# Kernel tuning notes

Measured on AMD Instinct MI355X. Metric: run time of the kernel, lower is better.

The kernel has to match this reference:

```python
import jax, jax.numpy as jnp
import numpy as np

HEADS = 16
LN_EPS = 1e-5


def setup_inputs() -> dict:
    key = jax.random.key(0)
    ks = jax.random.split(key, 4)
    B, S, C, U = 2, 2048, 1024, 1024
    scale = 1.0 / np.sqrt(C)
    return {
        "inputs": jax.random.normal(ks[0], (B, S, C), dtype=jnp.float32),
        "Wq": jax.random.normal(ks[1], (C, U), dtype=jnp.float32) * scale,
        "bq": jnp.zeros((U,), dtype=jnp.float32),
        "Wk": jax.random.normal(ks[2], (C, U), dtype=jnp.float32) * scale,
        "bk": jnp.zeros((U,), dtype=jnp.float32),
        "Wv": jax.random.normal(ks[3], (C, U), dtype=jnp.float32) * scale,
        "bv": jnp.zeros((U,), dtype=jnp.float32),
        "ln_gamma": jnp.ones((S, U), dtype=jnp.float32),
        "ln_beta": jnp.zeros((S, U), dtype=jnp.float32),
    }


def reference(inputs, Wq, bq, Wk, bk, Wv, bv, ln_gamma, ln_beta):
    B, S, C = inputs.shape
    U = Wq.shape[1]
    H = HEADS
    dh = U // H

    Q = inputs @ Wq + bq  # [B,S,U]
    K = inputs @ Wk + bk
    V = inputs @ Wv + bv

    # torch: concat(split(X, U//H, dim=-1), dim=0) -> head-major stacking on batch
    def split_heads(X):
        return jnp.moveaxis(X.reshape(B, S, H, dh), 2, 0).reshape(H * B, S, dh)

    Q_, K_, V_ = split_heads(Q), split_heads(K), split_heads(V)

    scores = jnp.einsum('bqd,bkd->bqk', Q_, K_) / jnp.sqrt(jnp.float32(dh))
    tri = jnp.tril(jnp.ones((S, S), dtype=bool))  # causal mask
    scores = jnp.where(tri[None, :, :], scores, jnp.float32(-1e9))
    attn = jax.nn.softmax(scores, axis=-1)
    out_ = jnp.einsum('bqk,bkd->bqd', attn, V_)  # [H*B,S,dh]

    # inverse: split on batch into H chunks of size B, concat on feature dim
    out = jnp.moveaxis(out_.reshape(H, B, S, dh), 0, 2).reshape(B, S, U)

    out = out + inputs  # residual

    # LayerNorm over normalized_shape=[S, U] (joint seq+feature stats)
    mu = jnp.mean(out, axis=(-2, -1), keepdims=True)
    var = jnp.mean(jnp.square(out - mu), axis=(-2, -1), keepdims=True)
    out = (out - mu) / jnp.sqrt(var + LN_EPS) * ln_gamma + ln_beta
    return out
```

## Files before the change

kernel.cpp:

```cpp
#include <hip/hip_runtime.h>
#include <hip/hip_bf16.h>


typedef __bf16 bf16_t;
typedef __bf16 bf16x8 __attribute__((ext_vector_type(8)));
typedef __bf16 bf16x4 __attribute__((ext_vector_type(4)));
typedef _Float16 f16_t;
typedef _Float16 f16x2 __attribute__((ext_vector_type(2)));
typedef _Float16 f16x4 __attribute__((ext_vector_type(4)));
typedef _Float16 f16x8 __attribute__((ext_vector_type(8)));
typedef float f32x4 __attribute__((ext_vector_type(4)));

constexpr int Bsz = 2;
constexpr int Seq = 2048;
constexpr int Cdim = 1024;
constexpr int Udim = 1024;
constexpr int Hn = 16;
constexpr int Dh = 64;
constexpr int Mrows = Bsz * Seq;
constexpr int PerBatch = Seq * Udim;
constexpr float SCLQ = 0.125f * 1.44269504088896340736f;

#if __has_builtin(__builtin_amdgcn_exp2f)
#define EXP2F(x) __builtin_amdgcn_exp2f(x)
#else
#define EXP2F(x) exp2f(x)
#endif

#define AINL __attribute__((always_inline))
#define BARRIER() __builtin_amdgcn_s_barrier()
#define SCHEDB() __builtin_amdgcn_sched_barrier(0)
#define WAITV4() asm volatile("s_waitcnt vmcnt(4)" ::: "memory")
#define WAITV0() asm volatile("s_waitcnt vmcnt(0)" ::: "memory")

__device__ __forceinline__ void gload16(const void* g, void* l)
{
    __builtin_amdgcn_global_load_lds(
        (const __attribute__((address_space(1))) void*)g,
        (__attribute__((address_space(3))) void*)l, 16, 0, 0);
}

__device__ __forceinline__ f16x2 pkrtz(float a, float b)
{
    return __builtin_bit_cast(f16x2, __builtin_amdgcn_cvt_pkrtz(a, b));
}

__global__ __launch_bounds__(256)
void prep(const float* __restrict__ X,
          const float* __restrict__ Wq, const float* __restrict__ Wk,
          const float* __restrict__ Wv,
          bf16_t* __restrict__ Xb,
          bf16_t* __restrict__ Tq, bf16_t* __restrict__ Tk,
          bf16_t* __restrict__ Tv, float* __restrict__ stats)
{
    int z = blockIdx.z;
    int tid = threadIdx.x;
    if (z < 3) {
        const float* W = (z == 0) ? Wq : (z == 1) ? Wk : Wv;
        bf16_t* T = (z == 0) ? Tq : (z == 1) ? Tk : Tv;
        __shared__ bf16_t t[64][65];
        int x0 = blockIdx.x * 64, y0 = blockIdx.y * 64;
        int tx = tid & 63, ty = tid >> 6;
        for (int i = ty; i < 64; i += 4)
            t[i][tx] = (bf16_t)W[(size_t)(y0 + i) * Cdim + x0 + tx];
        __syncthreads();
        for (int i = ty; i < 64; i += 4)
            T[(size_t)(x0 + i) * Cdim + y0 + tx] = t[tx][i];
    } else {
        int bi = blockIdx.y * 16 + blockIdx.x;
        if (bi == 0 && tid < 4) stats[tid] = 0.0f;
        const float4* Xv = (const float4*)X;
#pragma unroll
        for (int k = 0; k < 16; k++) {
            int i = bi * 4096 + k * 256 + tid;
            float4 v = Xv[i];
            bf16x4 o = { (bf16_t)v.x, (bf16_t)v.y, (bf16_t)v.z, (bf16_t)v.w };
            *(bf16x4*)(Xb + (size_t)i * 4) = o;
        }
    }
}

__global__ __launch_bounds__(256)
void gemm_qkv(const bf16_t* __restrict__ X,
              const bf16_t* __restrict__ Wt0, const bf16_t* __restrict__ Wt1,
              const bf16_t* __restrict__ Wt2,
              const float* __restrict__ b0, const float* __restrict__ b1,
              const float* __restrict__ b2,
              f16_t* __restrict__ O0, f16_t* __restrict__ O1, f16_t* __restrict__ O2v)
{
    int z = blockIdx.z;
    const bf16_t* Wt = (z == 0) ? Wt0 : (z == 1) ? Wt1 : Wt2;
    const float* bias = (z == 0) ? b0 : (z == 1) ? b1 : b2;
    float scl = (z == 0) ? SCLQ : 1.0f;

    constexpr int Kd = 1024, Nd = 1024;
    __shared__ __align__(16) bf16_t As[2][4096];
    __shared__ __align__(16) bf16_t Bs[2][4096];

    int tid = threadIdx.x;
    int wave = tid >> 6, lane = tid & 63, quad = lane >> 4, l16 = lane & 15;
    int wm = (wave & 1) * 64, wn = (wave >> 1) * 64;
    int m0 = blockIdx.y * 128, n0 = blockIdx.x * 128;

    f32x4 acc[4][4] = {};

    int e0 = wave * 512 + lane * 8;
    int r0 = e0 >> 5, c0 = e0 & 31;
    int e1 = e0 + 2048;
    int r1 = e1 >> 5, c1 = e1 & 31;
    const bf16_t* Ag = X + (size_t)m0 * Kd;
    const bf16_t* Bg = Wt + (size_t)n0 * Kd;

    auto STG = [&](int nb, int k0) AINL {
        gload16(Ag + (size_t)r0 * Kd + k0 + c0, &As[nb][wave * 512]);
        gload16(Ag + (size_t)r1 * Kd + k0 + c1, &As[nb][2048 + wave * 512]);
        gload16(Bg + (size_t)r0 * Kd + k0 + c0, &Bs[nb][wave * 512]);
        gload16(Bg + (size_t)r1 * Kd + k0 + c1, &Bs[nb][2048 + wave * 512]);
    };

    int kNext = 32;
    auto STEP = [&](int buf, bool doStage) AINL {
        BARRIER();
        if (doStage) { STG(buf ^ 1, kNext); kNext += 32; WAITV4(); }
        else WAITV0();
        BARRIER();
        SCHEDB();
        bf16x8 af[4], bfr[4];
#pragma unroll
        for (int i = 0; i < 4; i++)
            af[i] = *(const bf16x8*)&As[buf][(wm + i * 16 + l16) * 32 + quad * 8];
#pragma unroll
        for (int i = 0; i < 4; i++)
            bfr[i] = *(const bf16x8*)&Bs[buf][(wn + i * 16 + l16) * 32 + quad * 8];
#pragma unroll
        for (int mt = 0; mt < 4; mt++)
#pragma unroll
            for (int nt = 0; nt < 4; nt++)
                acc[mt][nt] = __builtin_amdgcn_mfma_f32_16x16x32_bf16(
                    af[mt], bfr[nt], acc[mt][nt], 0, 0, 0);
    };

    STG(0, 0);
    for (int it = 0; it < 15; it++) { STEP(0, true); STEP(1, true); }
    STEP(0, true);
    STEP(1, false);

    if (z < 2) {
        f16_t* Og = (z == 0) ? O0 : O1;
#pragma unroll
        for (int nt = 0; nt < 4; nt++) {
            int col = n0 + wn + nt * 16 + l16;
            float bv = bias[col];
#pragma unroll
            for (int mt = 0; mt < 4; mt++) {
                int row = m0 + wm + mt * 16 + quad * 4;
#pragma unroll
                for (int r = 0; r < 4; r++)
                    Og[(size_t)(row + r) * Nd + col] = (f16_t)((acc[mt][nt][r] + bv) * scl);
            }
        }
    } else {
        int bb = m0 >> 11;
#pragma unroll
        for (int nt = 0; nt < 4; nt++) {
            int col = n0 + wn + nt * 16 + l16;
            float bv = bias[col];
            int h = col >> 6, d = col & 63;
            f16_t* vbase = O2v + (((size_t)(bb * Hn + h) * Dh + d) << 11);
#pragma unroll
            for (int mt = 0; mt < 4; mt++) {
                int row = m0 + wm + mt * 16 + quad * 4;
                int s = row & (Seq - 1);
                f16x4 pk;
#pragma unroll
                for (int r = 0; r < 4; r++) pk[r] = (f16_t)(acc[mt][nt][r] + bv);
                *(f16x4*)(vbase + s) = pk;
            }
        }
    }
}

__global__ __launch_bounds__(512, 4)
void attn13(const f16_t* __restrict__ Q, const f16_t* __restrict__ K,
            const f16_t* __restrict__ Vt, const float* __restrict__ X,
            bf16_t* __restrict__ R, float* __restrict__ stats)
{
    int id = blockIdx.x;
    int c = id & 7;
    int rr = id >> 3;
    int g = rr & 3;
    int pi = rr >> 2;
    int bh = (g << 3) | c;
    int b = bh >> 4, h = bh & 15;
    int qa = 31 - pi, qb = pi, split = 15 - pi;

    int tid = threadIdx.x;
    int grp = tid >> 8;
    int w = (tid >> 6) & 3;
    int lane = tid & 63, quad = lane >> 4, l16 = lane & 15;
    size_t bS = (size_t)b * Seq;

    __shared__ __align__(16) char ldsRaw[65600];
    f16_t* KsBase = (f16_t*)(ldsRaw + grp * 32768);
    f16_t* VsBase = (f16_t*)(ldsRaw + grp * 32768 + 16384);
    float* cmbO   = (float*)(ldsRaw + 32768);
    float* cmbLS  = (float*)(ldsRaw + 49152);
    float* red    = (float*)(ldsRaw + 65536);

    const f16_t* Kg = K + bS * Udim + h * Dh;
    const f16_t* Vg = Vt + ((size_t)(b * Hn + h)) * Dh * Seq;

    int srow = w * 8 + (lane >> 3);
    int schunk = (lane & 7) ^ ((lane >> 3) & 7);

    int qidxA = qa * 64 + w * 16 + l16;
    int qidxB = qb * 64 + w * 16 + l16;
    const f16_t* QpA = Q + (bS + qidxA) * Udim + h * Dh;
    const f16_t* QpB = Q + (bS + qidxB) * Udim + h * Dh;
    f16x8 qfA[2], qfB[2];
#pragma unroll
    for (int s2 = 0; s2 < 2; s2++) {
        qfA[s2] = *(const f16x8*)(QpA + s2 * 32 + quad * 8);
        qfB[s2] = *(const f16x8*)(QpB + s2 * 32 + quad * 8);
    }

    int m = l16 & 7;
    int kO0 = l16 * 64 + ((quad ^ m) << 3);
    int kO1 = l16 * 64 + (((4 + quad) ^ m) << 3);
    int vO[4];
#pragma unroll
    for (int t = 0; t < 4; t++)
        vO[t] = l16 * 64 + (((t * 32 + quad * 8) ^ (m << 4)) >> 1);

    f32x4 OA[4] = {}, OB[4] = {};
    float lsA = 0.0f, lsB = 0.0f;

    auto STAGE = [&](int nb, int tl) AINL {
        const f16_t* kp = Kg + (size_t)(tl * 64 + srow) * Udim + schunk * 8;
        const f16_t* vp = Vg + (size_t)srow * Seq + tl * 64 + schunk * 8;
        f16_t* kd = KsBase + nb * 4096;
        f16_t* vd = VsBase + nb * 4096;
        gload16(kp, kd + w * 512);
        gload16(kp + (size_t)32 * Udim, kd + 2048 + w * 512);
        gload16(vp, vd + w * 512);
        gload16(vp + (size_t)32 * Seq, vd + 2048 + w * 512);
    };

    auto CN = [&](int buf, const f16x8 (&qf)[2], f32x4 (&O)[4], float& ls) AINL {
        const f16_t* Kb = KsBase + buf * 4096;
        const f16_t* Vb = VsBase + buf * 4096;
        f32x4 st[4];
#pragma unroll
        for (int t = 0; t < 4; t++) {
            f16x8 kf0 = *(const f16x8*)&Kb[kO0 + t * 1024];
            f16x8 kf1 = *(const f16x8*)&Kb[kO1 + t * 1024];
            f32x4 a = {};
            a = __builtin_amdgcn_mfma_f32_16x16x32_f16(kf0, qf[0], a, 0, 0, 0);
            a = __builtin_amdgcn_mfma_f32_16x16x32_f16(kf1, qf[1], a, 0, 0, 0);
            st[t] = a;
        }
        f16x4 pf[4];
#pragma unroll
        for (int t = 0; t < 4; t++) {
            float p0 = EXP2F(st[t][0]);
            float p1 = EXP2F(st[t][1]);
            float p2 = EXP2F(st[t][2]);
            float p3 = EXP2F(st[t][3]);
            ls += (p0 + p1) + (p2 + p3);
            f16x2 lo = pkrtz(p0, p1);
            f16x2 hi = pkrtz(p2, p3);
            pf[t][0] = lo[0]; pf[t][1] = lo[1];
            pf[t][2] = hi[0]; pf[t][3] = hi[1];
        }
#pragma unroll
        for (int t = 0; t < 4; t++)
#pragma unroll
            for (int dt = 0; dt < 4; dt++) {
                f16x4 vf = *(const f16x4*)&Vb[vO[t] + dt * 1024];
                O[dt] = __builtin_amdgcn_mfma_f32_16x16x16f16(vf, pf[t], O[dt], 0, 0, 0);
            }
    };

    auto CM = [&](int buf, const f16x8 (&qf)[2], f32x4 (&O)[4], float& ls,
                  int kv0, int qidx) AINL {
        const f16_t* Kb = KsBase + buf * 4096;
        const f16_t* Vb = VsBase + buf * 4096;
#pragma unroll
        for (int t = 0; t < 4; t++) {
            if (t <= w) {
                f16x8 kf0 = *(const f16x8*)&Kb[kO0 + t * 1024];
                f16x8 kf1 = *(const f16x8*)&Kb[kO1 + t * 1024];
                f32x4 a = {};
                a = __builtin_amdgcn_mfma_f32_16x16x32_f16(kf0, qf[0], a, 0, 0, 0);
                a = __builtin_amdgcn_mfma_f32_16x16x32_f16(kf1, qf[1], a, 0, 0, 0);
                f16x4 pfd;
#pragma unroll
                for (int r2 = 0; r2 < 4; r2++) {
                    float sv = a[r2];
                    if (kv0 + t * 16 + quad * 4 + r2 > qidx) sv = -1e30f;
                    float pv = EXP2F(sv);
                    ls += pv;
                    pfd[r2] = (f16_t)pv;
                }
#pragma unroll
                for (int dt = 0; dt < 4; dt++) {
                    f16x4 vf = *(const f16x4*)&Vb[vO[t] + dt * 1024];
                    O[dt] = __builtin_amdgcn_mfma_f32_16x16x16f16(vf, pfd, O[dt], 0, 0, 0);
                }
            }
        }
    };

    int r = 0;
    auto ROUND = [&](int buf) AINL {
        BARRIER();
        if (r < 16) {
            int rn = r + 1;
            int tl = (grp == 0) ? ((rn <= qb) ? rn : rn - qb - 1) : (split + rn);
            STAGE(buf ^ 1, tl);
            WAITV4();
        } else {
            WAITV0();
        }
        BARRIER();
        SCHEDB();
        if (grp == 0) {
            if (r < qb)       CN(buf, qfB, OB, lsB);
            else if (r == qb) CM(buf, qfB, OB, lsB, qb * 64, qidxB);
            else if (r < 16)  CN(buf, qfA, OA, lsA);
        } else {
            if (r < 16)       CN(buf, qfA, OA, lsA);
            else              CM(buf, qfA, OA, lsA, qa * 64, qidxA);
        }
        r++;
    };

    STAGE(0, (grp == 0) ? 0 : split);
    for (int i = 0; i < 8; i++) { ROUND(0); ROUND(1); }
    ROUND(0);

    BARRIER();

    lsA += __shfl_xor(lsA, 16);
    lsA += __shfl_xor(lsA, 32);

    float s_acc = 0.0f, ss_acc = 0.0f;

    if (grp == 1) {
        float* po = cmbO + w * 1024 + lane * 16;
#pragma unroll
        for (int dt = 0; dt < 4; dt++)
            *(f32x4*)(po + dt * 4) = OA[dt];
        if (lane < 16) cmbLS[w * 16 + l16] = lsA;
    } else {
        lsB += __shfl_xor(lsB, 16);
        lsB += __shfl_xor(lsB, 32);
        float invB = 1.0f / lsB;
        const float* XpB = X + (bS + qidxB) * Udim + h * Dh;
        bf16_t* RpB = R + (bS + qidxB) * Udim + h * Dh;
#pragma unroll
        for (int dt = 0; dt < 4; dt++) {
            f32x4 xv = *(const f32x4*)(XpB + dt * 16 + quad * 4);
            f32x4 o = OB[dt] * invB + xv;
            bf16x4 ob;
#pragma unroll
            for (int r2 = 0; r2 < 4; r2++) {
                ob[r2] = (bf16_t)o[r2];
                s_acc += o[r2];
                ss_acc += o[r2] * o[r2];
            }
            *(bf16x4*)(RpB + dt * 16 + quad * 4) = ob;
        }
    }
    __syncthreads();

    if (grp == 0) {
        const float* po = cmbO + w * 1024 + lane * 16;
#pragma unroll
        for (int dt = 0; dt < 4; dt++)
            OA[dt] += *(const f32x4*)(po + dt * 4);
        lsA += cmbLS[w * 16 + l16];
        float invA = 1.0f / lsA;
        const float* XpA = X + (bS + qidxA) * Udim + h * Dh;
        bf16_t* RpA = R + (bS + qidxA) * Udim + h * Dh;
#pragma unroll
        for (int dt = 0; dt < 4; dt++) {
            f32x4 xv = *(const f32x4*)(XpA + dt * 16 + quad * 4);
            f32x4 o = OA[dt] * invA + xv;
            bf16x4 ob;
#pragma unroll
            for (int r2 = 0; r2 < 4; r2++) {
                ob[r2] = (bf16_t)o[r2];
                s_acc += o[r2];
                ss_acc += o[r2] * o[r2];
            }
            *(bf16x4*)(RpA + dt * 16 + quad * 4) = ob;
        }
    }

#pragma unroll
    for (int o = 1; o < 64; o <<= 1) {
        s_acc += __shfl_xor(s_acc, o);
        ss_acc += __shfl_xor(ss_acc, o);
    }
    int w8 = tid >> 6;
    if (lane == 0) { red[w8] = s_acc; red[8 + w8] = ss_acc; }
    __syncthreads();
    if (tid == 0) {
        float s = 0.0f, ss = 0.0f;
#pragma unroll
        for (int i = 0; i < 8; i++) { s += red[i]; ss += red[8 + i]; }
        atomicAdd(&stats[b], s);
        atomicAdd(&stats[2 + b], ss);
    }
}

__global__ __launch_bounds__(256)
void ln_norm(const bf16_t* __restrict__ R, const float* __restrict__ gamma,
             const float* __restrict__ beta, const float* __restrict__ stats,
             float* __restrict__ out)
{
    constexpr float invN = 1.0f / (float)PerBatch;
    float mu[2], inv[2];
#pragma unroll
    for (int b = 0; b < 2; b++) {
        float m = stats[b] * invN;
        float var = stats[2 + b] * invN - m * m;
        mu[b] = m;
        inv[b] = rsqrtf(var + 1e-5f);
    }
    int i = blockIdx.x * 256 + threadIdx.x;
    int f = i * 8;
    int b = f >> 21;
    int su = f & (PerBatch - 1);
    bf16x8 rv = *(const bf16x8*)(R + f);
    float4 g0 = *(const float4*)(gamma + su);
    float4 g1 = *(const float4*)(gamma + su + 4);
    float4 be0 = *(const float4*)(beta + su);
    float4 be1 = *(const float4*)(beta + su + 4);
    float4 o0, o1;
    o0.x = ((float)rv[0] - mu[b]) * inv[b] * g0.x + be0.x;
    o0.y = ((float)rv[1] - mu[b]) * inv[b] * g0.y + be0.y;
    o0.z = ((float)rv[2] - mu[b]) * inv[b] * g0.z + be0.z;
    o0.w = ((float)rv[3] - mu[b]) * inv[b] * g0.w + be0.w;
    o1.x = ((float)rv[4] - mu[b]) * inv[b] * g1.x + be1.x;
    o1.y = ((float)rv[5] - mu[b]) * inv[b] * g1.y + be1.y;
    o1.z = ((float)rv[6] - mu[b]) * inv[b] * g1.z + be1.z;
    o1.w = ((float)rv[7] - mu[b]) * inv[b] * g1.w + be1.w;
    *(float4*)(out + f) = o0;
    *(float4*)(out + f + 4) = o1;
}

extern "C" void kernel_launch(void* const* d_in, const int* in_sizes, int n_in,
                              void* d_out, int out_size, void* d_ws, size_t ws_size,
                              hipStream_t stream)
{
    const float* X     = (const float*)d_in[0];
    const float* Wq    = (const float*)d_in[1];
    const float* bq    = (const float*)d_in[2];
    const float* Wk    = (const float*)d_in[3];
    const float* bk    = (const float*)d_in[4];
    const float* Wv    = (const float*)d_in[5];
    const float* bv    = (const float*)d_in[6];
    const float* gamma = (const float*)d_in[7];
    const float* beta  = (const float*)d_in[8];
    float* out = (float*)d_out;

    char* ws = (char*)d_ws;
    size_t off = 0;
    auto alloc = [&](size_t bytes) -> void* {
        void* p = ws + off;
        off += (bytes + 255) & ~(size_t)255;
        return p;
    };
    bf16_t* Xb = (bf16_t*)alloc((size_t)Mrows * Cdim * 2);
    bf16_t* Tq = (bf16_t*)alloc((size_t)Cdim * Udim * 2);
    bf16_t* Tk = (bf16_t*)alloc((size_t)Cdim * Udim * 2);
    bf16_t* Tv = (bf16_t*)alloc((size_t)Cdim * Udim * 2);
    f16_t*  Qb = (f16_t*)alloc((size_t)Mrows * Udim * 2);
    f16_t*  Kb = (f16_t*)alloc((size_t)Mrows * Udim * 2);
    f16_t*  Vtb = (f16_t*)alloc((size_t)Mrows * Udim * 2);
    bf16_t* Rb = (bf16_t*)alloc((size_t)Mrows * Udim * 2);
    float*  stats = (float*)alloc(4 * sizeof(float));

    prep<<<dim3(16, 16, 4), 256, 0, stream>>>(X, Wq, Wk, Wv, Xb, Tq, Tk, Tv, stats);
    gemm_qkv<<<dim3(8, 32, 3), 256, 0, stream>>>(Xb, Tq, Tk, Tv, bq, bk, bv, Qb, Kb, Vtb);
    attn13<<<dim3(512), 512, 0, stream>>>(Qb, Kb, Vtb, X, Rb, stats);
    ln_norm<<<dim3(2048), 256, 0, stream>>>(Rb, gamma, beta, stats, out);
}
```

Measured before the change: 184.0 us.

## Rebalance KV tile split between wave groups and share K/V tiles across two query blocks

The KV range for the paired query blocks is now split between the two 256-thread groups using a computed split point. This aims to even out the per-group round counts. Group 0 handles both query blocks on shared KV tiles through a new combined kernel (CN2), so each K/V fragment it loads feeds MFMAs for both queries. The round loop now runs a variable number of rounds with a single __syncthreads per round, replacing the explicit barrier/wait-count scheme. The combined path raises register pressure, and the waitcnt-based overlap of staging and compute may be weakened.

```diff
diff --git a/kernel.cpp b/kernel.cpp
--- a/kernel.cpp
+++ b/kernel.cpp
@@ -181,7 +181,7 @@
 }
 
 __global__ __launch_bounds__(512, 4)
-void attn13(const f16_t* __restrict__ Q, const f16_t* __restrict__ K,
+void attn14(const f16_t* __restrict__ Q, const f16_t* __restrict__ K,
             const f16_t* __restrict__ Vt, const float* __restrict__ X,
             bf16_t* __restrict__ R, float* __restrict__ stats)
 {
@@ -192,7 +192,13 @@
     int pi = rr >> 2;
     int bh = (g << 3) | c;
     int b = bh >> 4, h = bh & 15;
-    int qa = 31 - pi, qb = pi, split = 15 - pi;
+    int qa = 31 - pi, qb = pi;
+    int s0a = (32 - pi) >> 1;
+    int s0b = 31 - 2 * pi;
+    int s0 = (s0a < s0b) ? s0a : s0b;
+    int R0 = (qb + 1 > s0) ? qb + 1 : s0;
+    int R1 = qa + 1 - s0;
+    int Rn = (R0 > R1) ? R0 : R1;
 
     int tid = threadIdx.x;
     int grp = tid >> 8;
@@ -281,6 +287,55 @@
             }
     };
 
+    auto CN2 = [&](int buf) AINL {
+        const f16_t* Kb = KsBase + buf * 4096;
+        const f16_t* Vb = VsBase + buf * 4096;
+        f32x4 stA[4], stB[4];
+#pragma unroll
+        for (int t = 0; t < 4; t++) {
+            f16x8 kf0 = *(const f16x8*)&Kb[kO0 + t * 1024];
+            f16x8 kf1 = *(const f16x8*)&Kb[kO1 + t * 1024];
+            f32x4 a = {};
+            a = __builtin_amdgcn_mfma_f32_16x16x32_f16(kf0, qfA[0], a, 0, 0, 0);
+            a = __builtin_amdgcn_mfma_f32_16x16x32_f16(kf1, qfA[1], a, 0, 0, 0);
+            stA[t] = a;
+            f32x4 bb = {};
+            bb = __builtin_amdgcn_mfma_f32_16x16x32_f16(kf0, qfB[0], bb, 0, 0, 0);
+            bb = __builtin_amdgcn_mfma_f32_16x16x32_f16(kf1, qfB[1], bb, 0, 0, 0);
+            stB[t] = bb;
+        }
+        f16x4 pA[4], pB[4];
+#pragma unroll
+        for (int t = 0; t < 4; t++) {
+            float a0 = EXP2F(stA[t][0]);
+            float a1 = EXP2F(stA[t][1]);
+            float a2 = EXP2F(stA[t][2]);
+            float a3 = EXP2F(stA[t][3]);
+            lsA += (a0 + a1) + (a2 + a3);
+            f16x2 alo = pkrtz(a0, a1);
+            f16x2 ahi = pkrtz(a2, a3);
+            pA[t][0] = alo[0]; pA[t][1] = alo[1];
+            pA[t][2] = ahi[0]; pA[t][3] = ahi[1];
+            float b0 = EXP2F(stB[t][0]);
+            float b1 = EXP2F(stB[t][1]);
+            float b2 = EXP2F(stB[t][2]);
+            float b3 = EXP2F(stB[t][3]);
+            lsB += (b0 + b1) + (b2 + b3);
+            f16x2 blo = pkrtz(b0, b1);
+            f16x2 bhi = pkrtz(b2, b3);
+            pB[t][0] = blo[0]; pB[t][1] = blo[1];
+            pB[t][2] = bhi[0]; pB[t][3] = bhi[1];
+        }
+#pragma unroll
+        for (int t = 0; t < 4; t++)
+#pragma unroll
+            for (int dt = 0; dt < 4; dt++) {
+                f16x4 vf = *(const f16x4*)&Vb[vO[t] + dt * 1024];
+                OA[dt] = __builtin_amdgcn_mfma_f32_16x16x16f16(vf, pA[t], OA[dt], 0, 0, 0);
+                OB[dt] = __builtin_amdgcn_mfma_f32_16x16x16f16(vf, pB[t], OB[dt], 0, 0, 0);
+            }
+    };
+
     auto CM = [&](int buf, const f16x8 (&qf)[2], f32x4 (&O)[4], float& ls,
                   int kv0, int qidx) AINL {
         const f16_t* Kb = KsBase + buf * 4096;
@@ -311,35 +366,36 @@
         }
     };
 
-    int r = 0;
-    auto ROUND = [&](int buf) AINL {
-        BARRIER();
-        if (r < 16) {
-            int rn = r + 1;
-            int tl = (grp == 0) ? ((rn <= qb) ? rn : rn - qb - 1) : (split + rn);
-            STAGE(buf ^ 1, tl);
-            WAITV4();
+    auto ROUND = [&](int r, int buf) AINL {
+        if (grp == 0) {
+            if (r + 1 < R0) STAGE(buf ^ 1, r + 1);
+            bool aAct = (r < s0);
+            if (r < qb) {
+                if (aAct) CN2(buf);
+                else CN(buf, qfB, OB, lsB);
+            } else if (r == qb) {
+                if (aAct) CN(buf, qfA, OA, lsA);
+                CM(buf, qfB, OB, lsB, qb * 64, qidxB);
+            } else if (aAct) {
+                CN(buf, qfA, OA, lsA);
+            }
         } else {
-            WAITV0();
-        }
-        BARRIER();
-        SCHEDB();
-        if (grp == 0) {
-            if (r < qb)       CN(buf, qfB, OB, lsB);
-            else if (r == qb) CM(buf, qfB, OB, lsB, qb * 64, qidxB);
-            else if (r < 16)  CN(buf, qfA, OA, lsA);
-        } else {
-            if (r < 16)       CN(buf, qfA, OA, lsA);
-            else              CM(buf, qfA, OA, lsA, qa * 64, qidxA);
-        }
-        r++;
-    };
-
-    STAGE(0, (grp == 0) ? 0 : split);
-    for (int i = 0; i < 8; i++) { ROUND(0); ROUND(1); }
-    ROUND(0);
-
-    BARRIER();
+            if (r + 1 < R1) STAGE(buf ^ 1, s0 + r + 1);
+            if (r < R1) {
+                if (r == R1 - 1) CM(buf, qfA, OA, lsA, qa * 64, qidxA);
+                else CN(buf, qfA, OA, lsA);
+            }
+        }
+        __syncthreads();
+    };
+
+    STAGE(0, (grp == 0) ? 0 : s0);
+    __syncthreads();
+    {
+        int r = 0;
+        for (; r + 2 <= Rn; r += 2) { ROUND(r, 0); ROUND(r + 1, 1); }
+        if (r < Rn) ROUND(r, 0);
+    }
 
     lsA += __shfl_xor(lsA, 16);
     lsA += __shfl_xor(lsA, 32);
@@ -485,6 +541,6 @@
 
     prep<<<dim3(16, 16, 4), 256, 0, stream>>>(X, Wq, Wk, Wv, Xb, Tq, Tk, Tv, stats);
     gemm_qkv<<<dim3(8, 32, 3), 256, 0, stream>>>(Xb, Tq, Tk, Tv, bq, bk, bv, Qb, Kb, Vtb);
-    attn13<<<dim3(512), 512, 0, stream>>>(Qb, Kb, Vtb, X, Rb, stats);
+    attn14<<<dim3(512), 512, 0, stream>>>(Qb, Kb, Vtb, X, Rb, stats);
     ln_norm<<<dim3(2048), 256, 0, stream>>>(Rb, gamma, beta, stats, out);
 }
```

New measurement: 185.7 us. About the same (+0.9%).

## Software-pipeline QK^T and softmax-PV across rounds with split K/V staging

Applied to the files above, without the earlier changes.

Restructures the attention loop so each round computes QK^T for the current key tile while doing softmax and PV for the previous tile, ping-ponging score registers. K and V loads are staged separately, with V lagging K by one tile, and the explicit vmcnt waits plus one barrier per round are replaced by a single __syncthreads. The goal is to overlap MFMA work on QK with exp and PV and to cut barrier stalls. In exchange it holds more score registers live, which may raise register pressure at 512 threads and 4 waves per SIMD, and without explicit vmcnt waits the correctness of the LDS synchronisation rests on the compiler's waitcnt insertion before the barrier.

```diff
diff --git a/kernel.cpp b/kernel.cpp
--- a/kernel.cpp
+++ b/kernel.cpp
@@ -181,7 +181,7 @@
 }
 
 __global__ __launch_bounds__(512, 4)
-void attn13(const f16_t* __restrict__ Q, const f16_t* __restrict__ K,
+void attn15(const f16_t* __restrict__ Q, const f16_t* __restrict__ K,
             const f16_t* __restrict__ Vt, const float* __restrict__ X,
             bf16_t* __restrict__ R, float* __restrict__ stats)
 {
@@ -234,112 +234,106 @@
 
     f32x4 OA[4] = {}, OB[4] = {};
     float lsA = 0.0f, lsB = 0.0f;
-
-    auto STAGE = [&](int nb, int tl) AINL {
+    f32x4 stX[4], stY[4];
+
+    auto tl0 = [&](int rho) AINL -> int { return (rho <= qb) ? rho : rho - qb - 1; };
+
+    auto STAGE_K = [&](int nb, int tl) AINL {
         const f16_t* kp = Kg + (size_t)(tl * 64 + srow) * Udim + schunk * 8;
-        const f16_t* vp = Vg + (size_t)srow * Seq + tl * 64 + schunk * 8;
         f16_t* kd = KsBase + nb * 4096;
-        f16_t* vd = VsBase + nb * 4096;
         gload16(kp, kd + w * 512);
         gload16(kp + (size_t)32 * Udim, kd + 2048 + w * 512);
+    };
+    auto STAGE_V = [&](int nb, int tl) AINL {
+        const f16_t* vp = Vg + (size_t)srow * Seq + tl * 64 + schunk * 8;
+        f16_t* vd = VsBase + nb * 4096;
         gload16(vp, vd + w * 512);
         gload16(vp + (size_t)32 * Seq, vd + 2048 + w * 512);
     };
 
-    auto CN = [&](int buf, const f16x8 (&qf)[2], f32x4 (&O)[4], float& ls) AINL {
+    auto QK = [&](int buf, const f16x8 (&qf)[2], f32x4 (&sOUT)[4], int tcap) AINL {
         const f16_t* Kb = KsBase + buf * 4096;
-        const f16_t* Vb = VsBase + buf * 4096;
-        f32x4 st[4];
 #pragma unroll
         for (int t = 0; t < 4; t++) {
-            f16x8 kf0 = *(const f16x8*)&Kb[kO0 + t * 1024];
-            f16x8 kf1 = *(const f16x8*)&Kb[kO1 + t * 1024];
-            f32x4 a = {};
-            a = __builtin_amdgcn_mfma_f32_16x16x32_f16(kf0, qf[0], a, 0, 0, 0);
-            a = __builtin_amdgcn_mfma_f32_16x16x32_f16(kf1, qf[1], a, 0, 0, 0);
-            st[t] = a;
-        }
-        f16x4 pf[4];
-#pragma unroll
-        for (int t = 0; t < 4; t++) {
-            float p0 = EXP2F(st[t][0]);
-            float p1 = EXP2F(st[t][1]);
-            float p2 = EXP2F(st[t][2]);
-            float p3 = EXP2F(st[t][3]);
-            ls += (p0 + p1) + (p2 + p3);
-            f16x2 lo = pkrtz(p0, p1);
-            f16x2 hi = pkrtz(p2, p3);
-            pf[t][0] = lo[0]; pf[t][1] = lo[1];
-            pf[t][2] = hi[0]; pf[t][3] = hi[1];
-        }
-#pragma unroll
-        for (int t = 0; t < 4; t++)
-#pragma unroll
-            for (int dt = 0; dt < 4; dt++) {
-                f16x4 vf = *(const f16x4*)&Vb[vO[t] + dt * 1024];
-                O[dt] = __builtin_amdgcn_mfma_f32_16x16x16f16(vf, pf[t], O[dt], 0, 0, 0);
-            }
-    };
-
-    auto CM = [&](int buf, const f16x8 (&qf)[2], f32x4 (&O)[4], float& ls,
-                  int kv0, int qidx) AINL {
-        const f16_t* Kb = KsBase + buf * 4096;
-        const f16_t* Vb = VsBase + buf * 4096;
-#pragma unroll
-        for (int t = 0; t < 4; t++) {
-            if (t <= w) {
+            if (t <= tcap) {
                 f16x8 kf0 = *(const f16x8*)&Kb[kO0 + t * 1024];
                 f16x8 kf1 = *(const f16x8*)&Kb[kO1 + t * 1024];
                 f32x4 a = {};
                 a = __builtin_amdgcn_mfma_f32_16x16x32_f16(kf0, qf[0], a, 0, 0, 0);
                 a = __builtin_amdgcn_mfma_f32_16x16x32_f16(kf1, qf[1], a, 0, 0, 0);
-                f16x4 pfd;
+                sOUT[t] = a;
+            }
+        }
+    };
+
+    auto SMPV = [&](f32x4 (&sIN)[4], f32x4 (&O)[4], float& ls, bool msk,
+                    int kv0, int qidx, int tcap, int vbuf) AINL {
+        const f16_t* Vb = VsBase + vbuf * 4096;
+#pragma unroll
+        for (int t = 0; t < 4; t++) {
+            if (t <= tcap) {
+                float pv[4];
 #pragma unroll
                 for (int r2 = 0; r2 < 4; r2++) {
-                    float sv = a[r2];
-                    if (kv0 + t * 16 + quad * 4 + r2 > qidx) sv = -1e30f;
-                    float pv = EXP2F(sv);
-                    ls += pv;
-                    pfd[r2] = (f16_t)pv;
+                    float sv = sIN[t][r2];
+                    if (msk && (kv0 + t * 16 + quad * 4 + r2 > qidx)) sv = -1e30f;
+                    pv[r2] = EXP2F(sv);
+                    ls += pv[r2];
                 }
+                f16x2 lo = pkrtz(pv[0], pv[1]);
+                f16x2 hi = pkrtz(pv[2], pv[3]);
+                f16x4 pf;
+                pf[0] = lo[0]; pf[1] = lo[1]; pf[2] = hi[0]; pf[3] = hi[1];
 #pragma unroll
                 for (int dt = 0; dt < 4; dt++) {
                     f16x4 vf = *(const f16x4*)&Vb[vO[t] + dt * 1024];
-                    O[dt] = __builtin_amdgcn_mfma_f32_16x16x16f16(vf, pfd, O[dt], 0, 0, 0);
+                    O[dt] = __builtin_amdgcn_mfma_f32_16x16x16f16(vf, pf, O[dt], 0, 0, 0);
                 }
             }
         }
     };
 
-    int r = 0;
-    auto ROUND = [&](int buf) AINL {
-        BARRIER();
-        if (r < 16) {
-            int rn = r + 1;
-            int tl = (grp == 0) ? ((rn <= qb) ? rn : rn - qb - 1) : (split + rn);
-            STAGE(buf ^ 1, tl);
-            WAITV4();
+    auto ROUND = [&](int r, int buf, f32x4 (&sIN)[4], f32x4 (&sOUT)[4]) AINL {
+        if (grp == 0) {
+            if (r <= 14) STAGE_K(buf ^ 1, tl0(r + 1));
+            if (r <= 15) STAGE_V(buf ^ 1, tl0(r));
         } else {
-            WAITV0();
-        }
-        BARRIER();
-        SCHEDB();
+            if (r <= 15) STAGE_K(buf ^ 1, split + r + 1);
+            STAGE_V(buf ^ 1, split + r);
+        }
         if (grp == 0) {
-            if (r < qb)       CN(buf, qfB, OB, lsB);
-            else if (r == qb) CM(buf, qfB, OB, lsB, qb * 64, qidxB);
-            else if (r < 16)  CN(buf, qfA, OA, lsA);
+            if (r <= 15) {
+                if (r <= qb) QK(buf, qfB, sOUT, (r == qb) ? w : 3);
+                else         QK(buf, qfA, sOUT, 3);
+            }
         } else {
-            if (r < 16)       CN(buf, qfA, OA, lsA);
-            else              CM(buf, qfA, OA, lsA, qa * 64, qidxA);
-        }
-        r++;
-    };
-
-    STAGE(0, (grp == 0) ? 0 : split);
-    for (int i = 0; i < 8; i++) { ROUND(0); ROUND(1); }
-    ROUND(0);
-
-    BARRIER();
+            QK(buf, qfA, sOUT, (r == 16) ? w : 3);
+        }
+        if (r >= 1) {
+            if (grp == 0) {
+                if (r <= qb)          SMPV(sIN, OB, lsB, false, 0, 0, 3, buf);
+                else if (r == qb + 1) SMPV(sIN, OB, lsB, true, qb * 64, qidxB, w, buf);
+                else                  SMPV(sIN, OA, lsA, false, 0, 0, 3, buf);
+            } else {
+                SMPV(sIN, OA, lsA, false, 0, 0, 3, buf);
+            }
+        }
+        __syncthreads();
+    };
+
+    STAGE_K(0, (grp == 0) ? 0 : split);
+    __syncthreads();
+
+    for (int i = 0; i < 8; i++) {
+        ROUND(2 * i, 0, stX, stY);
+        ROUND(2 * i + 1, 1, stY, stX);
+    }
+    ROUND(16, 0, stX, stY);
+
+    if (grp == 1)
+        SMPV(stY, OA, lsA, true, qa * 64, qidxA, w, 1);
+
+    __syncthreads();
 
     lsA += __shfl_xor(lsA, 16);
     lsA += __shfl_xor(lsA, 32);
@@ -485,6 +479,6 @@
 
     prep<<<dim3(16, 16, 4), 256, 0, stream>>>(X, Wq, Wk, Wv, Xb, Tq, Tk, Tv, stats);
     gemm_qkv<<<dim3(8, 32, 3), 256, 0, stream>>>(Xb, Tq, Tk, Tv, bq, bk, bv, Qb, Kb, Vtb);
-    attn13<<<dim3(512), 512, 0, stream>>>(Qb, Kb, Vtb, X, Rb, stats);
+    attn15<<<dim3(512), 512, 0, stream>>>(Qb, Kb, Vtb, X, Rb, stats);
     ln_norm<<<dim3(2048), 256, 0, stream>>>(Rb, gamma, beta, stats, out);
 }
```

Result: slower. 197.1 us (+7.2%).
